# Kernel optimization log

Hardware: AMD Instinct MI355X
Metric: run time of the kernel (lower is better)

## Reference

```python
import jax, jax.numpy as jnp
import numpy as np

# ---- static config (matches init_kwargs) ----
B, NPG, C, L, H = 128, 256, 128, 3, 4   # graphs, nodes/graph, hidden, layers, heads
IN_CH, WALK, EDGE_IN, DEG = 30, 20, 11, 8
N = B * NPG
E = N * DEG
EPG = E // B                             # edges per graph
BN_EPS = 1e-5
HD = C // H


def setup_inputs() -> dict:
    key = jax.random.key(0)
    ks = list(jax.random.split(key, 80))
    ki = iter(ks)
    def w(shape, s=0.05):
        return jax.random.normal(next(ki), shape, jnp.float32) * s
    x = jax.random.normal(next(ki), (N, IN_CH), jnp.float32)
    # edges strictly within each graph (block-diagonal structure)
    src_l = jax.random.randint(next(ki), (E,), 0, NPG)
    dst_l = jax.random.randint(next(ki), (E,), 0, NPG)
    eg = jnp.repeat(jnp.arange(B, dtype=jnp.int32), EPG)
    edge_index = jnp.stack([eg * NPG + src_l.astype(jnp.int32),
                            eg * NPG + dst_l.astype(jnp.int32)])
    edge_attr = jax.random.normal(next(ki), (E, EDGE_IN), jnp.float32)
    batch = jnp.repeat(jnp.arange(B, dtype=jnp.int32), NPG)
    # all Linear weights stored [in, out] so y = x @ W + b
    inp = dict(x=x, edge_attr=edge_attr,
        in_W=w((IN_CH + WALK, C)), in_b=jnp.zeros((C,)),
        ep_W=w((EDGE_IN, C)), ep_b=jnp.zeros((C,)),
        ge_W=w((L, C, C)), ge_b=jnp.zeros((L, C)),          # GINE edge lin
        g1_W=w((L, C, C)), g1_b=jnp.zeros((L, C)),          # GINE nn layer1
        g2_W=w((L, C, C)), g2_b=jnp.zeros((L, C)),          # GINE nn layer2
        qkv_W=w((L, C, 3 * C)), qkv_b=jnp.zeros((L, 3 * C)),
        o_W=w((L, C, C)), o_b=jnp.zeros((L, C)),
        bn1_g=jnp.ones((L, C)), bn1_b=jnp.zeros((L, C)), bn1_m=w((L, C), 0.1), bn1_v=jnp.ones((L, C)),
        bn2_g=jnp.ones((L, C)), bn2_b=jnp.zeros((L, C)), bn2_m=w((L, C), 0.1), bn2_v=jnp.ones((L, C)),
        bn3_g=jnp.ones((L, C)), bn3_b=jnp.zeros((L, C)), bn3_m=w((L, C), 0.1), bn3_v=jnp.ones((L, C)),
        m1_W=w((L, C, 2 * C)), m1_b=jnp.zeros((L, 2 * C)),  # GPS ff block
        m2_W=w((L, 2 * C, C)), m2_b=jnp.zeros((L, C)),
        h1_W=w((C, 64)), h1_b=jnp.zeros((64,)),
        h2_W=w((64, 1)), h2_b=jnp.zeros((1,)),
        edge_index=edge_index, batch=batch)
    return inp


def _bn(x, g, b, m, v):  # BatchNorm1d, inference mode
    return (x - m) * jax.lax.rsqrt(v + BN_EPS) * g + b


def _rwse(edge_index):
    """diag of k-step random-walk matrix per graph; [N, WALK]."""
    src, dst = edge_index
    g = src // NPG
    A = jnp.zeros((B, NPG, NPG), jnp.float32).at[g, src % NPG, dst % NPG].add(1.0)
    A = A + jnp.eye(NPG, dtype=jnp.float32)          # add_self_loops
    deg = jnp.clip(jnp.sum(A, axis=-1), 1.0)         # out-degree of source
    M = jnp.swapaxes(A / deg[..., None], -1, -2)     # M[c,r] = A[r,c]/deg[r]
    p0 = jnp.broadcast_to(jnp.eye(NPG, dtype=jnp.float32), (B, NPG, NPG))
    def step(p, _):
        p = jnp.einsum('bcr,brn->bcn', M, p)
        return p, jnp.diagonal(p, axis1=-2, axis2=-1)
    _, diags = jax.lax.scan(step, p0, None, length=WALK)  # [WALK, B, NPG]
    return jnp.transpose(diags, (1, 2, 0)).reshape(N, WALK)


def _forward(x, edge_attr, in_W, in_b, ep_W, ep_b, ge_W, ge_b, g1_W, g1_b, g2_W, g2_b,
             qkv_W, qkv_b, o_W, o_b,
             bn1_g, bn1_b, bn1_m, bn1_v, bn2_g, bn2_b, bn2_m, bn2_v, bn3_g, bn3_b, bn3_m, bn3_v,
             m1_W, m1_b, m2_W, m2_b, h1_W, h1_b, h2_W, h2_b, edge_index, batch):
    pe = _rwse(edge_index)
    h = jnp.concatenate([x, pe], axis=-1) @ in_W + in_b      # input_proj
    e_emb = edge_attr @ ep_W + ep_b                          # edge_proj (dim==11)
    src, dst = edge_index[0], edge_index[1]
    for i in range(L):
        # --- GINEConv: relu(x_j + lin(edge)) -> scatter-sum -> MLP; eps=0 ---
        e = e_emb @ ge_W[i] + ge_b[i]
        msg = jax.nn.relu(h[src] + e)
        aggr = jax.ops.segment_sum(msg, dst, num_segments=N)
        loc = jax.nn.relu((h + aggr) @ g1_W[i] + g1_b[i]) @ g2_W[i] + g2_b[i]
        h1 = _bn(loc + h, bn1_g[i], bn1_b[i], bn1_m[i], bn1_v[i])
        # --- global multi-head attention on dense batch (uniform n, no padding) ---
        hd = h.reshape(B, NPG, C)
        qkv = hd @ qkv_W[i] + qkv_b[i]
        q, k, v = jnp.split(qkv, 3, axis=-1)
        q = q.reshape(B, NPG, H, HD); k = k.reshape(B, NPG, H, HD); v = v.reshape(B, NPG, H, HD)
        scores = jnp.einsum('bqhd,bkhd->bhqk', q, k) * (HD ** -0.5)
        attn = jax.nn.softmax(scores, axis=-1)
        o = jnp.einsum('bhqk,bkhd->bqhd', attn, v).reshape(B, NPG, C)
        o = (o @ o_W[i] + o_b[i]).reshape(N, C)
        h2 = _bn(o + h, bn2_g[i], bn2_b[i], bn2_m[i], bn2_v[i])
        # --- combine + feed-forward block ---
        out = h1 + h2
        ff = jax.nn.relu(out @ m1_W[i] + m1_b[i]) @ m2_W[i] + m2_b[i]
        h = _bn(out + ff, bn3_g[i], bn3_b[i], bn3_m[i], bn3_v[i])
    # --- global mean pool + head ---
    cnt = jax.ops.segment_sum(jnp.ones((N,), jnp.float32), batch, num_segments=B)
    pooled = jax.ops.segment_sum(h, batch, num_segments=B) / cnt[:, None]
    out = jax.nn.relu(pooled @ h1_W + h1_b) @ h2_W + h2_b
    return out[:, 0]  # [B]


def reference(x, edge_attr, in_W, in_b, ep_W, ep_b, ge_W, ge_b, g1_W, g1_b, g2_W, g2_b,
              qkv_W, qkv_b, o_W, o_b,
              bn1_g, bn1_b, bn1_m, bn1_v, bn2_g, bn2_b, bn2_m, bn2_v, bn3_g, bn3_b, bn3_m, bn3_v,
              m1_W, m1_b, m2_W, m2_b, h1_W, h1_b, h2_W, h2_b, edge_index, batch):
    return _forward(x, edge_attr, in_W, in_b, ep_W, ep_b, ge_W, ge_b, g1_W, g1_b, g2_W, g2_b,
                    qkv_W, qkv_b, o_W, o_b,
                    bn1_g, bn1_b, bn1_m, bn1_v, bn2_g, bn2_b, bn2_m, bn2_v, bn3_g, bn3_b, bn3_m, bn3_v,
                    m1_W, m1_b, m2_W, m2_b, h1_W, h1_b, h2_W, h2_b, edge_index, batch)
```

## Files before the change

### kernel.cpp

```cpp
#include <hip/hip_runtime.h>

#define GN   128
#define GP   256
#define NN   32768
#define NEDGE 262144
#define WALKN 20

typedef __attribute__((ext_vector_type(8))) short bfrag;
typedef __attribute__((ext_vector_type(4))) float ffrag;

__device__ __forceinline__ ushort f2b(float f){
  unsigned u = __float_as_uint(f);
  u += 0x7fffu + ((u >> 16) & 1u);
  return (ushort)(u >> 16);
}
__device__ __forceinline__ float b2f(ushort u){
  return __uint_as_float(((unsigned)u) << 16);
}
__device__ __forceinline__ unsigned addpair(unsigned a, unsigned b){
  float alo = __uint_as_float(a << 16), ahi = __uint_as_float(a & 0xffff0000u);
  float blo = __uint_as_float(b << 16), bhi = __uint_as_float(b & 0xffff0000u);
  return ((unsigned)f2b(ahi + bhi) << 16) | (unsigned)f2b(alo + blo);
}

__global__ __launch_bounds__(256) void build_edges(const int* __restrict__ ei, float* __restrict__ A,
                                                   int* __restrict__ epos, int* __restrict__ Ecnt){
  int e = blockIdx.x*256 + threadIdx.x;
  int s = ei[e], d = ei[NEDGE + e];
  int g = s >> 8;
  atomicAdd(&A[((size_t)g<<16) + ((size_t)(s&255)<<8) + (size_t)(d&255)], 1.0f);
  epos[e] = atomicAdd(&Ecnt[d], 1);
}

__global__ __launch_bounds__(256) void pack_edges(const int* __restrict__ ei, const float* __restrict__ ea,
                                                  const int* __restrict__ epos, float* __restrict__ pk){
  int e = blockIdx.x*256 + threadIdx.x;
  int d = ei[NEDGE + e];
  int pos = epos[e];
  if (pos >= 32) return;
  float* dst = pk + ((size_t)d*32 + pos)*12;
  dst[0] = __int_as_float(ei[e]);
  const float* s = ea + (size_t)e*11;
  #pragma unroll
  for (int t = 0; t < 11; t++) dst[1+t] = s[t];
}

__global__ __launch_bounds__(256) void rwse_deg(float* __restrict__ A, float* __restrict__ deg){
  int g = blockIdx.x, r = threadIdx.x;
  float* row = A + ((size_t)g<<16) + ((size_t)r<<8);
  row[r] += 1.0f;
  float s = 0.f;
  for (int c = 0; c < 256; c += 4){
    float4 v = *(const float4*)&row[c];
    s += v.x + v.y + v.z + v.w;
  }
  deg[(g<<8)+r] = fmaxf(s, 1.0f);
}

__global__ __launch_bounds__(256) void prep_m(const float* __restrict__ A, const float* __restrict__ deg,
                                              ushort* __restrict__ Mbf){
  __shared__ float As[64][65];
  __shared__ float Bs[64][65];
  __shared__ float invd[256];
  int g = blockIdx.x;
  const float* Ag = A + ((size_t)g<<16);
  int tid = threadIdx.x, tx = tid & 63, ty = tid >> 6;
  invd[tid] = 1.f / deg[(g<<8)+tid];
  ushort* Mg = Mbf + ((size_t)g<<16);
  const int pr[10] = {0,0,0,0,1,1,1,2,2,3};
  const int pc[10] = {0,1,2,3,1,2,3,2,3,3};
  for (int t = 0; t < 10; t++){
    int R0 = pr[t]*64, C0 = pc[t]*64;
    __syncthreads();
    #pragma unroll
    for (int i = 0; i < 16; i++){
      As[ty + i*4][tx] = Ag[(size_t)(R0 + ty + i*4)*256 + C0 + tx];
      Bs[ty + i*4][tx] = Ag[(size_t)(C0 + ty + i*4)*256 + R0 + tx];
    }
    __syncthreads();
    #pragma unroll
    for (int i = 0; i < 16; i++){
      int cl = ty + i*4;
      Mg[(size_t)(C0+cl)*256 + R0+tx] = f2b(As[tx][cl] * invd[R0+tx]);
      if (R0 != C0)
        Mg[(size_t)(R0+cl)*256 + C0+tx] = f2b(Bs[tx][cl] * invd[C0+tx]);
    }
  }
}

__global__ __launch_bounds__(256, 2) void rwse_mf(const ushort* __restrict__ Mbf,
                                                  float* __restrict__ pe){
  __shared__ __align__(16) ushort Pt[64*264];
  int bid = blockIdx.x;
  int g  = (bid & 7)*16 + (bid >> 5);
  int cb = ((bid >> 3) & 3) << 6;
  int tid = threadIdx.x, lane = tid & 63, w = tid >> 6;
  int l15 = lane & 15, quad = lane >> 4;
  const ushort* Mg = Mbf + ((size_t)g << 16);
  uint4 z4; z4.x = z4.y = z4.z = z4.w = 0u;
  for (int i = tid; i < 2112; i += 256) reinterpret_cast<uint4*>(Pt)[i] = z4;
  __syncthreads();
  if (tid < 64) Pt[tid*264 + cb + tid] = 0x3F80;
  __syncthreads();

  for (int s = 0; s < WALKN; s++){
    ffrag acc[4][4];
    #pragma unroll
    for (int mi = 0; mi < 4; mi++)
      #pragma unroll
      for (int n = 0; n < 4; n++) acc[mi][n] = (ffrag){0.f,0.f,0.f,0.f};
    for (int k0 = 0; k0 < 256; k0 += 32){
      bfrag a[4], b[4];
      #pragma unroll
      for (int mi = 0; mi < 4; mi++)
        a[mi] = *reinterpret_cast<const bfrag*>(&Mg[(size_t)(w*64 + mi*16 + l15)*256 + k0 + quad*8]);
      #pragma unroll
      for (int n = 0; n < 4; n++)
        b[n] = *reinterpret_cast<const bfrag*>(&Pt[(n*16 + l15)*264 + k0 + quad*8]);
      #pragma unroll
      for (int mi = 0; mi < 4; mi++)
        #pragma unroll
        for (int n = 0; n < 4; n++)
          acc[mi][n] = __builtin_amdgcn_mfma_f32_16x16x32_bf16(a[mi], b[n], acc[mi][n], 0, 0, 0);
    }
    __syncthreads();
    #pragma unroll
    for (int mi = 0; mi < 4; mi++){
      int rbase = w*64 + mi*16 + quad*4;
      #pragma unroll
      for (int n = 0; n < 4; n++){
        int cl = n*16 + l15;
        int dd = cb + cl - rbase;
        if (dd >= 0 && dd < 4){
          float dv = (dd==0)?acc[mi][n][0]:(dd==1)?acc[mi][n][1]:(dd==2)?acc[mi][n][2]:acc[mi][n][3];
          pe[(size_t)((g<<8) + cb + cl)*WALKN + s] = dv;
        }
        ushort4 pkk;
        pkk.x = f2b(acc[mi][n][0]); pkk.y = f2b(acc[mi][n][1]);
        pkk.z = f2b(acc[mi][n][2]); pkk.w = f2b(acc[mi][n][3]);
        *reinterpret_cast<ushort4*>(&Pt[cl*264 + rbase]) = pkk;
      }
    }
    __syncthreads();
  }
}

__global__ __launch_bounds__(256) void concat_kernel(const float* __restrict__ x, const float* __restrict__ pe,
                                                     ushort* __restrict__ xinb){
  int idx = blockIdx.x*256 + threadIdx.x;
  int row = idx >> 6, c = idx & 63;
  float v = 0.f;
  if (c < 30) v = x[(size_t)row*30 + c];
  else if (c < 50) v = pe[(size_t)row*20 + (c-30)];
  xinb[idx] = f2b(v);
}

__global__ __launch_bounds__(256) void prep_wt(const float* __restrict__ in_W, const float* __restrict__ g1_W,
                                               const float* __restrict__ g2_W, const float* __restrict__ qkv_W,
                                               const float* __restrict__ o_W, const float* __restrict__ m1_W,
                                               const float* __restrict__ m2_W, ushort* __restrict__ wt){
  int rgn = blockIdx.y;
  const float* src; int K, N, Kp; size_t dst;
  if (rgn == 0){ src = in_W; K=50; N=128; Kp=64; dst = 0; }
  else if (rgn <= 3){ int i=rgn-1;  src = g1_W + (size_t)i*16384; K=128; N=128; Kp=128; dst = 8192   + (size_t)i*16384; }
  else if (rgn <= 6){ int i=rgn-4;  src = g2_W + (size_t)i*16384; K=128; N=128; Kp=128; dst = 57344  + (size_t)i*16384; }
  else if (rgn <= 9){ int i=rgn-7;  src = qkv_W+ (size_t)i*49152; K=128; N=384; Kp=128; dst = 106496 + (size_t)i*49152; }
  else if (rgn <= 12){ int i=rgn-10; src = o_W  + (size_t)i*16384; K=128; N=128; Kp=128; dst = 253952 + (size_t)i*16384; }
  else if (rgn <= 15){ int i=rgn-13; src = m1_W + (size_t)i*32768; K=128; N=256; Kp=128; dst = 303104 + (size_t)i*32768; }
  else               { int i=rgn-16; src = m2_W + (size_t)i*32768; K=256; N=128; Kp=256; dst = 401408 + (size_t)i*32768; }
  int sz = N * Kp;
  int idx = blockIdx.x*256 + threadIdx.x;
  if (idx >= sz) return;
  int n = idx / Kp, kp = idx - n*Kp;
  float v = (kp < K) ? src[(size_t)kp*N + n] : 0.f;
  wt[dst + idx] = f2b(v);
}

template<int CINP>
__global__ __launch_bounds__(256, 2) void gemm_b(
    const ushort* __restrict__ X1, const ushort* __restrict__ WT,
    const float* __restrict__ bias, ushort* __restrict__ Y, int ldY, int colTiles)
{
  constexpr int XS = CINP + 8;
  __shared__ ushort XA[64 * XS];
  __shared__ ushort WS[128 * XS];
  int bt = blockIdx.x;
  int row0 = (bt / colTiles) * 64;
  int c0   = (bt % colTiles) * 128;
  int tid = threadIdx.x;
  int lane = tid & 63, wave = tid >> 6;
  int l15 = lane & 15, quad = lane >> 4;
  int wr = wave >> 1, wc = wave & 1;
  constexpr int C8 = CINP/8;

  #pragma unroll
  for (int it = 0; it < CINP/32; it++){
    int idx = tid + it*256;
    int r = idx / C8, c8 = (idx % C8)*8;
    *reinterpret_cast<uint4*>(&XA[r*XS + c8]) =
        *reinterpret_cast<const uint4*>(&X1[(size_t)(row0+r)*CINP + c8]);
  }
  #pragma unroll
  for (int it = 0; it < CINP/16; it++){
    int idx = tid + it*256;
    int n = idx / C8, c8 = (idx % C8)*8;
    *reinterpret_cast<uint4*>(&WS[n*XS + c8]) =
        *reinterpret_cast<const uint4*>(&WT[(size_t)(c0+n)*CINP + c8]);
  }
  __syncthreads();
  ffrag acc[2][4];
  #pragma unroll
  for (int m = 0; m < 2; m++)
    #pragma unroll
    for (int n = 0; n < 4; n++) acc[m][n] = (ffrag){0.f,0.f,0.f,0.f};
  #pragma unroll
  for (int ks = 0; ks < CINP/32; ks++){
    bfrag a[2], b[4];
    #pragma unroll
    for (int m = 0; m < 2; m++)
      a[m] = *reinterpret_cast<const bfrag*>(&XA[(32*wr + 16*m + l15)*XS + ks*32 + quad*8]);
    #pragma unroll
    for (int n = 0; n < 4; n++)
      b[n] = *reinterpret_cast<const bfrag*>(&WS[(64*wc + 16*n + l15)*XS + ks*32 + quad*8]);
    #pragma unroll
    for (int m = 0; m < 2; m++)
      #pragma unroll
      for (int n = 0; n < 4; n++)
        acc[m][n] = __builtin_amdgcn_mfma_f32_16x16x32_bf16(a[m], b[n], acc[m][n], 0, 0, 0);
  }
  #pragma unroll
  for (int m = 0; m < 2; m++)
    #pragma unroll
    for (int n = 0; n < 4; n++){
      int col = c0 + 64*wc + 16*n + l15;
      float bs = bias[col];
      #pragma unroll
      for (int rg = 0; rg < 4; rg++){
        int r = row0 + 32*wr + 16*m + quad*4 + rg;
        Y[(size_t)r*ldY + col] = f2b(acc[m][n][rg] + bs);
      }
    }
}

__global__ __launch_bounds__(256, 2) void gine_mlp(
    const ushort* __restrict__ hb, const ushort* __restrict__ agb,
    const ushort* __restrict__ w1, const float* __restrict__ b1v,
    const ushort* __restrict__ w2, const float* __restrict__ b2v,
    const float* __restrict__ bng, const float* __restrict__ bnb,
    const float* __restrict__ bnm, const float* __restrict__ bnv,
    ushort* __restrict__ h1b)
{
  __shared__ ushort XA[64*136];
  __shared__ ushort WS[128*136];
  __shared__ ushort T1[64*136];
  int row0 = blockIdx.x * 64;
  int tid = threadIdx.x, lane = tid & 63, wave = tid >> 6;
  int l15 = lane & 15, quad = lane >> 4;
  int wr = wave >> 1, wc = wave & 1;

  #pragma unroll
  for (int it = 0; it < 4; it++){
    int idx = tid + it*256;
    int r = idx >> 4, c8 = (idx & 15)*8;
    uint4 av = *reinterpret_cast<const uint4*>(&hb[(size_t)(row0+r)*128 + c8]);
    uint4 bv = *reinterpret_cast<const uint4*>(&agb[(size_t)(row0+r)*128 + c8]);
    uint4 o; o.x=addpair(av.x,bv.x); o.y=addpair(av.y,bv.y); o.z=addpair(av.z,bv.z); o.w=addpair(av.w,bv.w);
    *reinterpret_cast<uint4*>(&XA[r*136 + c8]) = o;
  }
  #pragma unroll
  for (int it = 0; it < 8; it++){
    int idx = tid + it*256;
    int n = idx >> 4, c8 = (idx & 15)*8;
    *reinterpret_cast<uint4*>(&WS[n*136 + c8]) =
        *reinterpret_cast<const uint4*>(&w1[(size_t)n*128 + c8]);
  }
  __syncthreads();
  ffrag acc[2][4];
  #pragma unroll
  for (int m = 0; m < 2; m++)
    #pragma unroll
    for (int n = 0; n < 4; n++) acc[m][n] = (ffrag){0.f,0.f,0.f,0.f};
  #pragma unroll
  for (int ks = 0; ks < 4; ks++){
    bfrag a[2], b[4];
    #pragma unroll
    for (int m = 0; m < 2; m++)
      a[m] = *reinterpret_cast<const bfrag*>(&XA[(32*wr + 16*m + l15)*136 + ks*32 + quad*8]);
    #pragma unroll
    for (int n = 0; n < 4; n++)
      b[n] = *reinterpret_cast<const bfrag*>(&WS[(64*wc + 16*n + l15)*136 + ks*32 + quad*8]);
    #pragma unroll
    for (int m = 0; m < 2; m++)
      #pragma unroll
      for (int n = 0; n < 4; n++)
        acc[m][n] = __builtin_amdgcn_mfma_f32_16x16x32_bf16(a[m], b[n], acc[m][n], 0, 0, 0);
  }
  __syncthreads();
  #pragma unroll
  for (int m = 0; m < 2; m++)
    #pragma unroll
    for (int n = 0; n < 4; n++){
      int col = 64*wc + 16*n + l15;
      float bs = b1v[col];
      #pragma unroll
      for (int rg = 0; rg < 4; rg++){
        int rl = 32*wr + 16*m + quad*4 + rg;
        T1[rl*136 + col] = f2b(fmaxf(acc[m][n][rg] + bs, 0.f));
      }
    }
  #pragma unroll
  for (int it = 0; it < 8; it++){
    int idx = tid + it*256;
    int n = idx >> 4, c8 = (idx & 15)*8;
    *reinterpret_cast<uint4*>(&WS[n*136 + c8]) =
        *reinterpret_cast<const uint4*>(&w2[(size_t)n*128 + c8]);
  }
  __syncthreads();
  #pragma unroll
  for (int m = 0; m < 2; m++)
    #pragma unroll
    for (int n = 0; n < 4; n++) acc[m][n] = (ffrag){0.f,0.f,0.f,0.f};
  #pragma unroll
  for (int ks = 0; ks < 4; ks++){
    bfrag a[2], b[4];
    #pragma unroll
    for (int m = 0; m < 2; m++)
      a[m] = *reinterpret_cast<const bfrag*>(&T1[(32*wr + 16*m + l15)*136 + ks*32 + quad*8]);
    #pragma unroll
    for (int n = 0; n < 4; n++)
      b[n] = *reinterpret_cast<const bfrag*>(&WS[(64*wc + 16*n + l15)*136 + ks*32 + quad*8]);
    #pragma unroll
    for (int m = 0; m < 2; m++)
      #pragma unroll
      for (int n = 0; n < 4; n++)
        acc[m][n] = __builtin_amdgcn_mfma_f32_16x16x32_bf16(a[m], b[n], acc[m][n], 0, 0, 0);
  }
  #pragma unroll
  for (int m = 0; m < 2; m++)
    #pragma unroll
    for (int n = 0; n < 4; n++){
      int col = 64*wc + 16*n + l15;
      float bs = b2v[col];
      float sc = rsqrtf(bnv[col] + 1e-5f) * bng[col];
      float sh = bnb[col] - bnm[col]*sc;
      #pragma unroll
      for (int rg = 0; rg < 4; rg++){
        int r = row0 + 32*wr + 16*m + quad*4 + rg;
        float v = acc[m][n][rg] + bs + b2f(hb[(size_t)r*128 + col]);
        h1b[(size_t)r*128 + col] = f2b(v*sc + sh);
      }
    }
}

__global__ __launch_bounds__(256, 1) void ff_fused(
    const ushort* __restrict__ obb, const ushort* __restrict__ hb, const ushort* __restrict__ h1b,
    const ushort* __restrict__ wo, const float* __restrict__ ob_b,
    const float* __restrict__ bn2g, const float* __restrict__ bn2b,
    const float* __restrict__ bn2m, const float* __restrict__ bn2v,
    const ushort* __restrict__ wm1, const float* __restrict__ m1b,
    const ushort* __restrict__ wm2, const float* __restrict__ m2b,
    const float* __restrict__ bn3g, const float* __restrict__ bn3b,
    const float* __restrict__ bn3m, const float* __restrict__ bn3v,
    ushort* __restrict__ hout)
{
  __shared__ ushort XA[64*136];
  __shared__ ushort WS[256*136];
  __shared__ ushort OUT[64*136];
  __shared__ ushort T2[64*264];
  int row0 = blockIdx.x * 64;
  int tid = threadIdx.x, lane = tid & 63, wave = tid >> 6;
  int l15 = lane & 15, quad = lane >> 4;
  int wr = wave >> 1, wc = wave & 1;

  #pragma unroll
  for (int it = 0; it < 4; it++){
    int idx = tid + it*256;
    int r = idx >> 4, c8 = (idx & 15)*8;
    *reinterpret_cast<uint4*>(&XA[r*136 + c8]) =
        *reinterpret_cast<const uint4*>(&obb[(size_t)(row0+r)*128 + c8]);
  }
  #pragma unroll
  for (int it = 0; it < 8; it++){
    int idx = tid + it*256;
    int n = idx >> 4, c8 = (idx & 15)*8;
    *reinterpret_cast<uint4*>(&WS[n*136 + c8]) =
        *reinterpret_cast<const uint4*>(&wo[(size_t)n*128 + c8]);
  }
  __syncthreads();
  ffrag acc[2][4];
  #pragma unroll
  for (int m = 0; m < 2; m++)
    #pragma unroll
    for (int n = 0; n < 4; n++) acc[m][n] = (ffrag){0.f,0.f,0.f,0.f};
  #pragma unroll
  for (int ks = 0; ks < 4; ks++){
    bfrag a[2], b[4];
    #pragma unroll
    for (int m = 0; m < 2; m++)
      a[m] = *reinterpret_cast<const bfrag*>(&XA[(32*wr + 16*m + l15)*136 + ks*32 + quad*8]);
    #pragma unroll
    for (int n = 0; n < 4; n++)
      b[n] = *reinterpret_cast<const bfrag*>(&WS[(64*wc + 16*n + l15)*136 + ks*32 + quad*8]);
    #pragma unroll
    for (int m = 0; m < 2; m++)
      #pragma unroll
      for (int n = 0; n < 4; n++)
        acc[m][n] = __builtin_amdgcn_mfma_f32_16x16x32_bf16(a[m], b[n], acc[m][n], 0, 0, 0);
  }
  __syncthreads();
  #pragma unroll
  for (int m = 0; m < 2; m++)
    #pragma unroll
    for (int n = 0; n < 4; n++){
      int col = 64*wc + 16*n + l15;
      float bs = ob_b[col];
      float sc = rsqrtf(bn2v[col] + 1e-5f) * bn2g[col];
      float sh = bn2b[col] - bn2m[col]*sc;
      #pragma unroll
      for (int rg = 0; rg < 4; rg++){
        int rl = 32*wr + 16*m + quad*4 + rg;
        int r = row0 + rl;
        float v = acc[m][n][rg] + bs + b2f(hb[(size_t)r*128 + col]);
        v = v*sc + sh + b2f(h1b[(size_t)r*128 + col]);
        OUT[rl*136 + col] = f2b(v);
      }
    }
  #pragma unroll
  for (int it = 0; it < 16; it++){
    int idx = tid + it*256;
    int n = idx >> 4, c8 = (idx & 15)*8;
    *reinterpret_cast<uint4*>(&WS[n*136 + c8]) =
        *reinterpret_cast<const uint4*>(&wm1[(size_t)n*128 + c8]);
  }
  __syncthreads();
  ffrag acc2[2][8];
  #pragma unroll
  for (int m = 0; m < 2; m++)
    #pragma unroll
    for (int n = 0; n < 8; n++) acc2[m][n] = (ffrag){0.f,0.f,0.f,0.f};
  #pragma unroll
  for (int ks = 0; ks < 4; ks++){
    bfrag a[2], b[8];
    #pragma unroll
    for (int m = 0; m < 2; m++)
      a[m] = *reinterpret_cast<const bfrag*>(&OUT[(32*wr + 16*m + l15)*136 + ks*32 + quad*8]);
    #pragma unroll
    for (int n = 0; n < 8; n++)
      b[n] = *reinterpret_cast<const bfrag*>(&WS[(128*wc + 16*n + l15)*136 + ks*32 + quad*8]);
    #pragma unroll
    for (int m = 0; m < 2; m++)
      #pragma unroll
      for (int n = 0; n < 8; n++)
        acc2[m][n] = __builtin_amdgcn_mfma_f32_16x16x32_bf16(a[m], b[n], acc2[m][n], 0, 0, 0);
  }
  __syncthreads();
  #pragma unroll
  for (int m = 0; m < 2; m++)
    #pragma unroll
    for (int n = 0; n < 8; n++){
      int col = 128*wc + 16*n + l15;
      float bs = m1b[col];
      #pragma unroll
      for (int rg = 0; rg < 4; rg++){
        int rl = 32*wr + 16*m + quad*4 + rg;
        T2[rl*264 + col] = f2b(fmaxf(acc2[m][n][rg] + bs, 0.f));
      }
    }
  #pragma unroll
  for (int it = 0; it < 16; it++){
    int idx = tid + it*256;
    int n = idx >> 5, c8 = (idx & 31)*8;
    *reinterpret_cast<uint4*>(&WS[n*264 + c8]) =
        *reinterpret_cast<const uint4*>(&wm2[(size_t)n*256 + c8]);
  }
  __syncthreads();
  #pragma unroll
  for (int m = 0; m < 2; m++)
    #pragma unroll
    for (int n = 0; n < 4; n++) acc[m][n] = (ffrag){0.f,0.f,0.f,0.f};
  #pragma unroll
  for (int ks = 0; ks < 8; ks++){
    bfrag a[2], b[4];
    #pragma unroll
    for (int m = 0; m < 2; m++)
      a[m] = *reinterpret_cast<const bfrag*>(&T2[(32*wr + 16*m + l15)*264 + ks*32 + quad*8]);
    #pragma unroll
    for (int n = 0; n < 4; n++)
      b[n] = *reinterpret_cast<const bfrag*>(&WS[(64*wc + 16*n + l15)*264 + ks*32 + quad*8]);
    #pragma unroll
    for (int m = 0; m < 2; m++)
      #pragma unroll
      for (int n = 0; n < 4; n++)
        acc[m][n] = __builtin_amdgcn_mfma_f32_16x16x32_bf16(a[m], b[n], acc[m][n], 0, 0, 0);
  }
  #pragma unroll
  for (int m = 0; m < 2; m++)
    #pragma unroll
    for (int n = 0; n < 4; n++){
      int col = 64*wc + 16*n + l15;
      float bs = m2b[col];
      float sc = rsqrtf(bn3v[col] + 1e-5f) * bn3g[col];
      float sh = bn3b[col] - bn3m[col]*sc;
      #pragma unroll
      for (int rg = 0; rg < 4; rg++){
        int rl = 32*wr + 16*m + quad*4 + rg;
        float v = acc[m][n][rg] + bs + b2f(OUT[rl*136 + col]);
        hout[(size_t)(row0+rl)*128 + col] = f2b(v*sc + sh);
      }
    }
}

__global__ __launch_bounds__(256) void wp_all(const float* __restrict__ epW, const float* __restrict__ epb,
                                              const float* __restrict__ geW, const float* __restrict__ geb,
                                              float* __restrict__ Wp, float* __restrict__ bp){
  int i = blockIdx.x;
  const float* gw = geW + (size_t)i*16384;
  float* wp = Wp + (size_t)i*1408;
  int tid = threadIdx.x;
  for (int idx = tid; idx < 1408; idx += 256){
    int t = idx >> 7, c = idx & 127;
    float s = 0.f;
    for (int k = 0; k < 128; k++) s += epW[t*128+k] * gw[(size_t)k*128 + c];
    wp[idx] = s;
  }
  if (tid < 128){
    float s = geb[(size_t)i*128 + tid];
    for (int k = 0; k < 128; k++) s += epb[k] * gw[(size_t)k*128 + tid];
    bp[(size_t)i*128 + tid] = s;
  }
}

__global__ __launch_bounds__(256) void gine_aggr2(const ushort* __restrict__ hb, const float* __restrict__ pk,
                                                  const int* __restrict__ Ecnt,
                                                  const float* __restrict__ Wp, const float* __restrict__ bp,
                                                  ushort* __restrict__ agb){
  int n = blockIdx.x*2 + (threadIdx.x >> 7);
  int ch = threadIdx.x & 127;
  int cnt = Ecnt[n]; if (cnt > 32) cnt = 32;
  float wreg[11];
  #pragma unroll
  for (int t = 0; t < 11; t++) wreg[t] = Wp[t*128 + ch];
  float bpc = bp[ch];
  const float* pkn = pk + (size_t)n*384;
  float acc = 0.f;
  int j = 0;
  for (; j + 4 <= cnt; j += 4){
    const float* p0 = pkn + (size_t)(j+0)*12;
    const float* p1 = pkn + (size_t)(j+1)*12;
    const float* p2 = pkn + (size_t)(j+2)*12;
    const float* p3 = pkn + (size_t)(j+3)*12;
    int s0 = __float_as_int(p0[0]), s1 = __float_as_int(p1[0]);
    int s2 = __float_as_int(p2[0]), s3 = __float_as_int(p3[0]);
    float h0 = b2f(hb[(size_t)s0*128 + ch]);
    float h1 = b2f(hb[(size_t)s1*128 + ch]);
    float h2 = b2f(hb[(size_t)s2*128 + ch]);
    float h3 = b2f(hb[(size_t)s3*128 + ch]);
    float e0 = bpc, e1 = bpc, e2 = bpc, e3 = bpc;
    #pragma unroll
    for (int t = 0; t < 11; t++){
      e0 += p0[1+t]*wreg[t]; e1 += p1[1+t]*wreg[t];
      e2 += p2[1+t]*wreg[t]; e3 += p3[1+t]*wreg[t];
    }
    acc += fmaxf(h0+e0, 0.f) + fmaxf(h1+e1, 0.f) + fmaxf(h2+e2, 0.f) + fmaxf(h3+e3, 0.f);
  }
  for (; j < cnt; j++){
    const float* p0 = pkn + (size_t)j*12;
    int s0 = __float_as_int(p0[0]);
    float h0 = b2f(hb[(size_t)s0*128 + ch]);
    float e0 = bpc;
    #pragma unroll
    for (int t = 0; t < 11; t++) e0 += p0[1+t]*wreg[t];
    acc += fmaxf(h0+e0, 0.f);
  }
  agb[(size_t)n*128 + ch] = f2b(acc);
}

__global__ __launch_bounds__(256, 2) void attn_mf(const ushort* __restrict__ qkvb, ushort* __restrict__ obb){
  __shared__ ushort Ks[256 * 40];
  __shared__ ushort Vt[32 * 264];
  __shared__ ushort PA[4 * 16 * 264];
  int g = blockIdx.x >> 2, hh = blockIdx.x & 3;
  int tid = threadIdx.x, lane = tid & 63, w = tid >> 6;
  int l15 = lane & 15, quad = lane >> 4;
  const ushort* base = qkvb + (size_t)(g<<8)*384;

  #pragma unroll
  for (int it = 0; it < 4; it++){
    int idx = tid + it*256;
    int key = idx >> 2, d8 = (idx & 3)*8;
    uint4 kv = *reinterpret_cast<const uint4*>(&base[(size_t)key*384 + 128 + hh*32 + d8]);
    *reinterpret_cast<uint4*>(&Ks[key*40 + d8]) = kv;
    uint4 vv = *reinterpret_cast<const uint4*>(&base[(size_t)key*384 + 256 + hh*32 + d8]);
    const ushort* vp = reinterpret_cast<const ushort*>(&vv);
    #pragma unroll
    for (int t = 0; t < 8; t++) Vt[(d8+t)*264 + key] = vp[t];
  }
  bfrag qf[4];
  #pragma unroll
  for (int qg = 0; qg < 4; qg++){
    int q = w*64 + qg*16 + l15;
    qf[qg] = *reinterpret_cast<const bfrag*>(&base[(size_t)q*384 + hh*32 + quad*8]);
  }
  __syncthreads();

  ushort* pw = &PA[w * 16 * 264];
  const float sc_ = 0.17677669529663687f;
  for (int qg = 0; qg < 4; qg++){
    ffrag sc[16];
    #pragma unroll
    for (int kg = 0; kg < 16; kg++){
      bfrag bk = *reinterpret_cast<const bfrag*>(&Ks[(kg*16 + l15)*40 + quad*8]);
      ffrag z = (ffrag){0.f,0.f,0.f,0.f};
      sc[kg] = __builtin_amdgcn_mfma_f32_16x16x32_bf16(qf[qg], bk, z, 0, 0, 0);
    }
    float inv_l[4];
    #pragma unroll
    for (int rg = 0; rg < 4; rg++){
      float m = sc[0][rg];
      #pragma unroll
      for (int kg = 1; kg < 16; kg++) m = fmaxf(m, sc[kg][rg]);
      #pragma unroll
      for (int off = 1; off < 16; off <<= 1) m = fmaxf(m, __shfl_xor(m, off, 16));
      float ssum = 0.f;
      #pragma unroll
      for (int kg = 0; kg < 16; kg++){
        float p = __expf((sc[kg][rg] - m) * sc_);
        sc[kg][rg] = p; ssum += p;
      }
      #pragma unroll
      for (int off = 1; off < 16; off <<= 1) ssum += __shfl_xor(ssum, off, 16);
      inv_l[rg] = 1.f / ssum;
    }
    #pragma unroll
    for (int kg = 0; kg < 16; kg++)
      #pragma unroll
      for (int rg = 0; rg < 4; rg++)
        pw[(quad*4 + rg)*264 + kg*16 + l15] = f2b(sc[kg][rg]);
    ffrag oa[2];
    oa[0] = (ffrag){0.f,0.f,0.f,0.f};
    oa[1] = (ffrag){0.f,0.f,0.f,0.f};
    #pragma unroll
    for (int ks = 0; ks < 8; ks++){
      bfrag pa = *reinterpret_cast<const bfrag*>(&pw[l15*264 + ks*32 + quad*8]);
      #pragma unroll
      for (int n16 = 0; n16 < 2; n16++){
        bfrag bv = *reinterpret_cast<const bfrag*>(&Vt[(n16*16 + l15)*264 + ks*32 + quad*8]);
        oa[n16] = __builtin_amdgcn_mfma_f32_16x16x32_bf16(pa, bv, oa[n16], 0, 0, 0);
      }
    }
    #pragma unroll
    for (int n16 = 0; n16 < 2; n16++)
      #pragma unroll
      for (int rg = 0; rg < 4; rg++){
        int q = w*64 + qg*16 + quad*4 + rg;
        int col = hh*32 + n16*16 + l15;
        obb[((size_t)(g<<8) + q)*128 + col] = f2b(oa[n16][rg] * inv_l[rg]);
      }
  }
}

__global__ __launch_bounds__(256) void head_kernel(const ushort* __restrict__ hb,
                                                   const float* __restrict__ W1, const float* __restrict__ b1,
                                                   const float* __restrict__ W2, const float* __restrict__ b2,
                                                   float* __restrict__ out){
  int g = blockIdx.x, tid = threadIdx.x;
  int c = tid & 127, half = tid >> 7;
  __shared__ float part[2][128];
  __shared__ float pool[128];
  __shared__ float hid[64];
  float s = 0.f;
  for (int n = half*128; n < half*128 + 128; n++)
    s += b2f(hb[(size_t)((g<<8)+n)*128 + c]);
  part[half][c] = s;
  __syncthreads();
  if (tid < 128) pool[tid] = (part[0][tid] + part[1][tid]) * (1.f/256.f);
  __syncthreads();
  if (tid < 64){
    float v = b1[tid];
    for (int k = 0; k < 128; k++) v += pool[k] * W1[k*64 + tid];
    hid[tid] = fmaxf(v, 0.f);
  }
  __syncthreads();
  if (tid == 0){
    float v = b2[0];
    for (int k = 0; k < 64; k++) v += hid[k] * W2[k];
    out[g] = v;
  }
}

extern "C" void kernel_launch(void* const* d_in, const int* in_sizes, int n_in,
                              void* d_out, int out_size, void* d_ws, size_t ws_size,
                              hipStream_t stream){
  (void)in_sizes; (void)n_in; (void)out_size; (void)ws_size;
  const float* x      = (const float*)d_in[0];
  const float* eattr  = (const float*)d_in[1];
  const float* in_W   = (const float*)d_in[2];
  const float* in_b   = (const float*)d_in[3];
  const float* ep_W   = (const float*)d_in[4];
  const float* ep_b   = (const float*)d_in[5];
  const float* ge_W   = (const float*)d_in[6];
  const float* ge_b   = (const float*)d_in[7];
  const float* g1_W   = (const float*)d_in[8];
  const float* g1_b   = (const float*)d_in[9];
  const float* g2_W   = (const float*)d_in[10];
  const float* g2_b   = (const float*)d_in[11];
  const float* qkv_W  = (const float*)d_in[12];
  const float* qkv_b  = (const float*)d_in[13];
  const float* o_W    = (const float*)d_in[14];
  const float* o_b    = (const float*)d_in[15];
  const float* bn1g = (const float*)d_in[16]; const float* bn1b = (const float*)d_in[17];
  const float* bn1m = (const float*)d_in[18]; const float* bn1v = (const float*)d_in[19];
  const float* bn2g = (const float*)d_in[20]; const float* bn2b = (const float*)d_in[21];
  const float* bn2m = (const float*)d_in[22]; const float* bn2v = (const float*)d_in[23];
  const float* bn3g = (const float*)d_in[24]; const float* bn3b = (const float*)d_in[25];
  const float* bn3m = (const float*)d_in[26]; const float* bn3v = (const float*)d_in[27];
  const float* m1_W = (const float*)d_in[28]; const float* m1_b = (const float*)d_in[29];
  const float* m2_W = (const float*)d_in[30]; const float* m2_b = (const float*)d_in[31];
  const float* h1_W = (const float*)d_in[32]; const float* h1_b = (const float*)d_in[33];
  const float* h2_W = (const float*)d_in[34]; const float* h2_b = (const float*)d_in[35];
  const int*   ei   = (const int*)d_in[36];
  float* out = (float*)d_out;
  float* ws  = (float*)d_ws;
  int*   wsi = (int*)d_ws;

  const size_t oA    = 0;
  const size_t oMbf  = 8388608;
  const size_t oPk   = 12582912;
  const size_t oDeg  = 25165824;
  const size_t oPe   = 25198592;
  const size_t oHb   = 25853952;
  const size_t oH1b  = 27951104;
  const size_t oBb   = 30048256;
  const size_t oWp   = 32145408;
  const size_t oBp   = 32149632;
  const size_t oEpos = 32150016;
  const size_t oEcnt = 32412160;
  const size_t oWT   = 32444928;
  ushort* wt   = (ushort*)(ws + oWT);
  ushort* mbf  = (ushort*)(ws + oMbf);
  ushort* xinb = (ushort*)(ws + 0);
  ushort* qkvb = (ushort*)(ws + 0);
  ushort* hb   = (ushort*)(ws + oHb);
  ushort* h1b  = (ushort*)(ws + oH1b);
  ushort* bbuf = (ushort*)(ws + oBb);

  hipMemsetAsync(ws + oA, 0, 8388608*sizeof(float), stream);
  hipMemsetAsync(wsi + oEcnt, 0, 32768*sizeof(int), stream);
  build_edges<<<NEDGE/256, 256, 0, stream>>>(ei, ws+oA, wsi+oEpos, wsi+oEcnt);
  pack_edges<<<NEDGE/256, 256, 0, stream>>>(ei, eattr, wsi+oEpos, ws+oPk);
  rwse_deg<<<GN, 256, 0, stream>>>(ws+oA, ws+oDeg);
  prep_m<<<GN, 256, 0, stream>>>(ws+oA, ws+oDeg, mbf);
  rwse_mf<<<GN*4, 256, 0, stream>>>(mbf, ws+oPe);

  prep_wt<<<dim3(192, 19), 256, 0, stream>>>(in_W, g1_W, g2_W, qkv_W, o_W, m1_W, m2_W, wt);

  concat_kernel<<<NN*64/256, 256, 0, stream>>>(x, ws+oPe, xinb);
  gemm_b<64><<<512, 256, 0, stream>>>(xinb, wt + 0, in_b, hb, 128, 1);

  wp_all<<<3, 256, 0, stream>>>(ep_W, ep_b, ge_W, ge_b, ws+oWp, ws+oBp);

  for (int i = 0; i < 3; i++){
    gine_aggr2<<<NN/2, 256, 0, stream>>>(hb, ws+oPk, wsi+oEcnt,
                                         ws+oWp + (size_t)i*1408, ws+oBp + (size_t)i*128, bbuf);
    gine_mlp<<<512, 256, 0, stream>>>(hb, bbuf,
        wt + 8192 + (size_t)i*16384, g1_b + (size_t)i*128,
        wt + 57344 + (size_t)i*16384, g2_b + (size_t)i*128,
        bn1g+(size_t)i*128, bn1b+(size_t)i*128, bn1m+(size_t)i*128, bn1v+(size_t)i*128,
        h1b);
    gemm_b<128><<<1536, 256, 0, stream>>>(hb, wt + 106496 + (size_t)i*49152,
                                          qkv_b + (size_t)i*384, qkvb, 384, 3);
    attn_mf<<<GN*4, 256, 0, stream>>>(qkvb, bbuf);
    ff_fused<<<512, 256, 0, stream>>>(bbuf, hb, h1b,
        wt + 253952 + (size_t)i*16384, o_b + (size_t)i*128,
        bn2g+(size_t)i*128, bn2b+(size_t)i*128, bn2m+(size_t)i*128, bn2v+(size_t)i*128,
        wt + 303104 + (size_t)i*32768, m1_b + (size_t)i*256,
        wt + 401408 + (size_t)i*32768, m2_b + (size_t)i*128,
        bn3g+(size_t)i*128, bn3b+(size_t)i*128, bn3m+(size_t)i*128, bn3v+(size_t)i*128,
        hb);
  }

  head_kernel<<<GN, 256, 0, stream>>>(hb, h1_W, h1_b, h2_W, h2_b, out);
}
```

Baseline: 737.7 us.

## Stage per-graph node features in LDS for GINE aggregation and fuse degree prep

GINE aggregation now runs one block per half-graph. Each block first copies the graph's 256x128 bf16 node features into shared memory, so neighbour gathers hit LDS instead of scattered global reads. Each thread handles two channels, reads the packed edge records with float4 loads, and processes two edges per iteration. The degree computation is also folded into the M-matrix prep kernel, which drops one launch and the degree buffer round trip. The cost is 64KB of shared memory per block and a much smaller grid (256 blocks), which lowers parallelism and occupancy. Each block also loads the whole graph's features even though it only produces half of the destination nodes.

```diff
diff --git a/kernel.cpp b/kernel.cpp
--- a/kernel.cpp
+++ b/kernel.cpp
@@ -45,27 +45,23 @@
   for (int t = 0; t < 11; t++) dst[1+t] = s[t];
 }
 
-__global__ __launch_bounds__(256) void rwse_deg(float* __restrict__ A, float* __restrict__ deg){
-  int g = blockIdx.x, r = threadIdx.x;
-  float* row = A + ((size_t)g<<16) + ((size_t)r<<8);
-  row[r] += 1.0f;
-  float s = 0.f;
-  for (int c = 0; c < 256; c += 4){
-    float4 v = *(const float4*)&row[c];
-    s += v.x + v.y + v.z + v.w;
-  }
-  deg[(g<<8)+r] = fmaxf(s, 1.0f);
-}
-
-__global__ __launch_bounds__(256) void prep_m(const float* __restrict__ A, const float* __restrict__ deg,
-                                              ushort* __restrict__ Mbf){
+__global__ __launch_bounds__(256) void prep_m2(float* __restrict__ A, ushort* __restrict__ Mbf){
   __shared__ float As[64][65];
   __shared__ float Bs[64][65];
   __shared__ float invd[256];
   int g = blockIdx.x;
-  const float* Ag = A + ((size_t)g<<16);
+  float* Ag = A + ((size_t)g<<16);
   int tid = threadIdx.x, tx = tid & 63, ty = tid >> 6;
-  invd[tid] = 1.f / deg[(g<<8)+tid];
+  {
+    float* row = Ag + ((size_t)tid<<8);
+    row[tid] += 1.0f;
+    float s = 0.f;
+    for (int c = 0; c < 256; c += 4){
+      float4 v = *(const float4*)&row[c];
+      s += v.x + v.y + v.z + v.w;
+    }
+    invd[tid] = 1.f / fmaxf(s, 1.0f);
+  }
   ushort* Mg = Mbf + ((size_t)g<<16);
   const int pr[10] = {0,0,0,0,1,1,1,2,2,3};
   const int pc[10] = {0,1,2,3,1,2,3,2,3,3};
@@ -530,49 +526,74 @@
   }
 }
 
-__global__ __launch_bounds__(256) void gine_aggr2(const ushort* __restrict__ hb, const float* __restrict__ pk,
-                                                  const int* __restrict__ Ecnt,
-                                                  const float* __restrict__ Wp, const float* __restrict__ bp,
-                                                  ushort* __restrict__ agb){
-  int n = blockIdx.x*2 + (threadIdx.x >> 7);
-  int ch = threadIdx.x & 127;
-  int cnt = Ecnt[n]; if (cnt > 32) cnt = 32;
-  float wreg[11];
-  #pragma unroll
-  for (int t = 0; t < 11; t++) wreg[t] = Wp[t*128 + ch];
-  float bpc = bp[ch];
-  const float* pkn = pk + (size_t)n*384;
-  float acc = 0.f;
-  int j = 0;
-  for (; j + 4 <= cnt; j += 4){
-    const float* p0 = pkn + (size_t)(j+0)*12;
-    const float* p1 = pkn + (size_t)(j+1)*12;
-    const float* p2 = pkn + (size_t)(j+2)*12;
-    const float* p3 = pkn + (size_t)(j+3)*12;
-    int s0 = __float_as_int(p0[0]), s1 = __float_as_int(p1[0]);
-    int s2 = __float_as_int(p2[0]), s3 = __float_as_int(p3[0]);
-    float h0 = b2f(hb[(size_t)s0*128 + ch]);
-    float h1 = b2f(hb[(size_t)s1*128 + ch]);
-    float h2 = b2f(hb[(size_t)s2*128 + ch]);
-    float h3 = b2f(hb[(size_t)s3*128 + ch]);
-    float e0 = bpc, e1 = bpc, e2 = bpc, e3 = bpc;
-    #pragma unroll
-    for (int t = 0; t < 11; t++){
-      e0 += p0[1+t]*wreg[t]; e1 += p1[1+t]*wreg[t];
-      e2 += p2[1+t]*wreg[t]; e3 += p3[1+t]*wreg[t];
-    }
-    acc += fmaxf(h0+e0, 0.f) + fmaxf(h1+e1, 0.f) + fmaxf(h2+e2, 0.f) + fmaxf(h3+e3, 0.f);
-  }
-  for (; j < cnt; j++){
-    const float* p0 = pkn + (size_t)j*12;
-    int s0 = __float_as_int(p0[0]);
-    float h0 = b2f(hb[(size_t)s0*128 + ch]);
-    float e0 = bpc;
-    #pragma unroll
-    for (int t = 0; t < 11; t++) e0 += p0[1+t]*wreg[t];
-    acc += fmaxf(h0+e0, 0.f);
-  }
-  agb[(size_t)n*128 + ch] = f2b(acc);
+__global__ __launch_bounds__(256, 2) void gine_aggr3(
+    const ushort* __restrict__ hb, const float* __restrict__ pk,
+    const int* __restrict__ Ecnt,
+    const float* __restrict__ Wp, const float* __restrict__ bp,
+    ushort* __restrict__ agb)
+{
+  __shared__ ushort Hs[256*128];
+  int g = blockIdx.x >> 1;
+  int half = blockIdx.x & 1;
+  int tid = threadIdx.x;
+  const ushort* hg = hb + ((size_t)(g<<8))*128;
+  #pragma unroll
+  for (int it = 0; it < 16; it++){
+    int idx = tid + it*256;
+    reinterpret_cast<uint4*>(Hs)[idx] = reinterpret_cast<const uint4*>(hg)[idx];
+  }
+  int sub = tid >> 6;
+  int cp  = tid & 63;
+  float w0[11], w1[11];
+  #pragma unroll
+  for (int t = 0; t < 11; t++){ w0[t] = Wp[t*128 + cp*2]; w1[t] = Wp[t*128 + cp*2 + 1]; }
+  float bp0 = bp[cp*2], bp1 = bp[cp*2 + 1];
+  __syncthreads();
+
+  for (int d0 = 0; d0 < 128; d0 += 4){
+    int dst = (g<<8) + half*128 + d0 + sub;
+    int cnt = Ecnt[dst]; if (cnt > 32) cnt = 32;
+    float a0 = 0.f, a1 = 0.f;
+    const float4* pr = reinterpret_cast<const float4*>(pk + (size_t)dst*384);
+    int j = 0;
+    for (; j + 2 <= cnt; j += 2){
+      float4 q0 = pr[j*3+0], q1 = pr[j*3+1], q2 = pr[j*3+2];
+      float4 r0 = pr[j*3+3], r1 = pr[j*3+4], r2 = pr[j*3+5];
+      int sA = __float_as_int(q0.x) & 255;
+      int sB = __float_as_int(r0.x) & 255;
+      unsigned hA = *reinterpret_cast<const unsigned*>(&Hs[sA*128 + cp*2]);
+      unsigned hB = *reinterpret_cast<const unsigned*>(&Hs[sB*128 + cp*2]);
+      float eA0 = bp0 + q0.y*w0[0] + q0.z*w0[1] + q0.w*w0[2]
+                + q1.x*w0[3] + q1.y*w0[4] + q1.z*w0[5] + q1.w*w0[6]
+                + q2.x*w0[7] + q2.y*w0[8] + q2.z*w0[9] + q2.w*w0[10];
+      float eA1 = bp1 + q0.y*w1[0] + q0.z*w1[1] + q0.w*w1[2]
+                + q1.x*w1[3] + q1.y*w1[4] + q1.z*w1[5] + q1.w*w1[6]
+                + q2.x*w1[7] + q2.y*w1[8] + q2.z*w1[9] + q2.w*w1[10];
+      float eB0 = bp0 + r0.y*w0[0] + r0.z*w0[1] + r0.w*w0[2]
+                + r1.x*w0[3] + r1.y*w0[4] + r1.z*w0[5] + r1.w*w0[6]
+                + r2.x*w0[7] + r2.y*w0[8] + r2.z*w0[9] + r2.w*w0[10];
+      float eB1 = bp1 + r0.y*w1[0] + r0.z*w1[1] + r0.w*w1[2]
+                + r1.x*w1[3] + r1.y*w1[4] + r1.z*w1[5] + r1.w*w1[6]
+                + r2.x*w1[7] + r2.y*w1[8] + r2.z*w1[9] + r2.w*w1[10];
+      a0 += fmaxf(eA0 + b2f((ushort)hA), 0.f) + fmaxf(eB0 + b2f((ushort)hB), 0.f);
+      a1 += fmaxf(eA1 + b2f((ushort)(hA >> 16)), 0.f) + fmaxf(eB1 + b2f((ushort)(hB >> 16)), 0.f);
+    }
+    for (; j < cnt; j++){
+      float4 q0 = pr[j*3+0], q1 = pr[j*3+1], q2 = pr[j*3+2];
+      int sA = __float_as_int(q0.x) & 255;
+      unsigned hA = *reinterpret_cast<const unsigned*>(&Hs[sA*128 + cp*2]);
+      float eA0 = bp0 + q0.y*w0[0] + q0.z*w0[1] + q0.w*w0[2]
+                + q1.x*w0[3] + q1.y*w0[4] + q1.z*w0[5] + q1.w*w0[6]
+                + q2.x*w0[7] + q2.y*w0[8] + q2.z*w0[9] + q2.w*w0[10];
+      float eA1 = bp1 + q0.y*w1[0] + q0.z*w1[1] + q0.w*w1[2]
+                + q1.x*w1[3] + q1.y*w1[4] + q1.z*w1[5] + q1.w*w1[6]
+                + q2.x*w1[7] + q2.y*w1[8] + q2.z*w1[9] + q2.w*w1[10];
+      a0 += fmaxf(eA0 + b2f((ushort)hA), 0.f);
+      a1 += fmaxf(eA1 + b2f((ushort)(hA >> 16)), 0.f);
+    }
+    unsigned o = ((unsigned)f2b(a1) << 16) | (unsigned)f2b(a0);
+    *reinterpret_cast<unsigned*>(&agb[(size_t)dst*128 + cp*2]) = o;
+  }
 }
 
 __global__ __launch_bounds__(256, 2) void attn_mf(const ushort* __restrict__ qkvb, ushort* __restrict__ obb){
@@ -726,7 +747,6 @@
   const size_t oA    = 0;
   const size_t oMbf  = 8388608;
   const size_t oPk   = 12582912;
-  const size_t oDeg  = 25165824;
   const size_t oPe   = 25198592;
   const size_t oHb   = 25853952;
   const size_t oH1b  = 27951104;
@@ -748,8 +768,7 @@
   hipMemsetAsync(wsi + oEcnt, 0, 32768*sizeof(int), stream);
   build_edges<<<NEDGE/256, 256, 0, stream>>>(ei, ws+oA, wsi+oEpos, wsi+oEcnt);
   pack_edges<<<NEDGE/256, 256, 0, stream>>>(ei, eattr, wsi+oEpos, ws+oPk);
-  rwse_deg<<<GN, 256, 0, stream>>>(ws+oA, ws+oDeg);
-  prep_m<<<GN, 256, 0, stream>>>(ws+oA, ws+oDeg, mbf);
+  prep_m2<<<GN, 256, 0, stream>>>(ws+oA, mbf);
   rwse_mf<<<GN*4, 256, 0, stream>>>(mbf, ws+oPe);
 
   prep_wt<<<dim3(192, 19), 256, 0, stream>>>(in_W, g1_W, g2_W, qkv_W, o_W, m1_W, m2_W, wt);
@@ -760,7 +779,7 @@
   wp_all<<<3, 256, 0, stream>>>(ep_W, ep_b, ge_W, ge_b, ws+oWp, ws+oBp);
 
   for (int i = 0; i < 3; i++){
-    gine_aggr2<<<NN/2, 256, 0, stream>>>(hb, ws+oPk, wsi+oEcnt,
+    gine_aggr3<<<GN*2, 256, 0, stream>>>(hb, ws+oPk, wsi+oEcnt,
                                          ws+oWp + (size_t)i*1408, ws+oBp + (size_t)i*128, bbuf);
     gine_mlp<<<512, 256, 0, stream>>>(hb, bbuf,
         wt + 8192 + (size_t)i*16384, g1_b + (size_t)i*128,
```

New measurement: 799.8 us. 8.4% more time.

## Fuse edge build/pack, degree/prep, concat/input GEMM; widen RWSE tiles

Applied to the files above, without the earlier changes.

Merges edge counting and packing into one kernel, folds the degree computation into the transition-matrix prep, and fuses the feature concat into a dedicated input GEMM. The random-walk MFMA kernel now uses 512-thread blocks covering 128 columns, halving the re-reads of M per graph. This removes several launches and intermediate buffers. The larger LDS footprint and register use in the RWSE kernel may lower occupancy.

```diff
diff --git a/kernel.cpp b/kernel.cpp
--- a/kernel.cpp
+++ b/kernel.cpp
@@ -23,49 +23,40 @@
   return ((unsigned)f2b(ahi + bhi) << 16) | (unsigned)f2b(alo + blo);
 }
 
-__global__ __launch_bounds__(256) void build_edges(const int* __restrict__ ei, float* __restrict__ A,
-                                                   int* __restrict__ epos, int* __restrict__ Ecnt){
+__global__ __launch_bounds__(256) void build_pack(const int* __restrict__ ei, const float* __restrict__ ea,
+                                                  float* __restrict__ A, int* __restrict__ Ecnt,
+                                                  float* __restrict__ pk){
   int e = blockIdx.x*256 + threadIdx.x;
   int s = ei[e], d = ei[NEDGE + e];
   int g = s >> 8;
   atomicAdd(&A[((size_t)g<<16) + ((size_t)(s&255)<<8) + (size_t)(d&255)], 1.0f);
-  epos[e] = atomicAdd(&Ecnt[d], 1);
-}
-
-__global__ __launch_bounds__(256) void pack_edges(const int* __restrict__ ei, const float* __restrict__ ea,
-                                                  const int* __restrict__ epos, float* __restrict__ pk){
-  int e = blockIdx.x*256 + threadIdx.x;
-  int d = ei[NEDGE + e];
-  int pos = epos[e];
-  if (pos >= 32) return;
-  float* dst = pk + ((size_t)d*32 + pos)*12;
-  dst[0] = __int_as_float(ei[e]);
-  const float* s = ea + (size_t)e*11;
-  #pragma unroll
-  for (int t = 0; t < 11; t++) dst[1+t] = s[t];
-}
-
-__global__ __launch_bounds__(256) void rwse_deg(float* __restrict__ A, float* __restrict__ deg){
-  int g = blockIdx.x, r = threadIdx.x;
-  float* row = A + ((size_t)g<<16) + ((size_t)r<<8);
-  row[r] += 1.0f;
-  float s = 0.f;
-  for (int c = 0; c < 256; c += 4){
-    float4 v = *(const float4*)&row[c];
-    s += v.x + v.y + v.z + v.w;
-  }
-  deg[(g<<8)+r] = fmaxf(s, 1.0f);
-}
-
-__global__ __launch_bounds__(256) void prep_m(const float* __restrict__ A, const float* __restrict__ deg,
-                                              ushort* __restrict__ Mbf){
+  int pos = atomicAdd(&Ecnt[d], 1);
+  if (pos < 32){
+    float* dst = pk + ((size_t)d*32 + pos)*12;
+    dst[0] = __int_as_float(s);
+    const float* src = ea + (size_t)e*11;
+    #pragma unroll
+    for (int t = 0; t < 11; t++) dst[1+t] = src[t];
+  }
+}
+
+__global__ __launch_bounds__(256) void prep_m2(float* __restrict__ A, ushort* __restrict__ Mbf){
   __shared__ float As[64][65];
   __shared__ float Bs[64][65];
   __shared__ float invd[256];
   int g = blockIdx.x;
-  const float* Ag = A + ((size_t)g<<16);
+  float* Ag = A + ((size_t)g<<16);
   int tid = threadIdx.x, tx = tid & 63, ty = tid >> 6;
-  invd[tid] = 1.f / deg[(g<<8)+tid];
+  {
+    float* row = Ag + ((size_t)tid<<8);
+    row[tid] += 1.0f;
+    float s = 0.f;
+    for (int c = 0; c < 256; c += 4){
+      float4 v = *(const float4*)&row[c];
+      s += v.x + v.y + v.z + v.w;
+    }
+    invd[tid] = 1.f / fmaxf(s, 1.0f);
+  }
   ushort* Mg = Mbf + ((size_t)g<<16);
   const int pr[10] = {0,0,0,0,1,1,1,2,2,3};
   const int pc[10] = {0,1,2,3,1,2,3,2,3,3};
@@ -88,47 +79,47 @@
   }
 }
 
-__global__ __launch_bounds__(256, 2) void rwse_mf(const ushort* __restrict__ Mbf,
+__global__ __launch_bounds__(512, 4) void rwse_mf(const ushort* __restrict__ Mbf,
                                                   float* __restrict__ pe){
-  __shared__ __align__(16) ushort Pt[64*264];
+  __shared__ __align__(16) ushort Pt[128*264];
   int bid = blockIdx.x;
-  int g  = (bid & 7)*16 + (bid >> 5);
-  int cb = ((bid >> 3) & 3) << 6;
+  int g  = (bid & 7)*16 + (bid >> 4);
+  int cb = ((bid >> 3) & 1) << 7;
   int tid = threadIdx.x, lane = tid & 63, w = tid >> 6;
   int l15 = lane & 15, quad = lane >> 4;
   const ushort* Mg = Mbf + ((size_t)g << 16);
   uint4 z4; z4.x = z4.y = z4.z = z4.w = 0u;
-  for (int i = tid; i < 2112; i += 256) reinterpret_cast<uint4*>(Pt)[i] = z4;
-  __syncthreads();
-  if (tid < 64) Pt[tid*264 + cb + tid] = 0x3F80;
+  for (int i = tid; i < 4224; i += 512) reinterpret_cast<uint4*>(Pt)[i] = z4;
+  __syncthreads();
+  if (tid < 128) Pt[tid*264 + cb + tid] = 0x3F80;
   __syncthreads();
 
   for (int s = 0; s < WALKN; s++){
-    ffrag acc[4][4];
-    #pragma unroll
-    for (int mi = 0; mi < 4; mi++)
-      #pragma unroll
-      for (int n = 0; n < 4; n++) acc[mi][n] = (ffrag){0.f,0.f,0.f,0.f};
+    ffrag acc[2][8];
+    #pragma unroll
+    for (int mi = 0; mi < 2; mi++)
+      #pragma unroll
+      for (int n = 0; n < 8; n++) acc[mi][n] = (ffrag){0.f,0.f,0.f,0.f};
     for (int k0 = 0; k0 < 256; k0 += 32){
-      bfrag a[4], b[4];
-      #pragma unroll
-      for (int mi = 0; mi < 4; mi++)
-        a[mi] = *reinterpret_cast<const bfrag*>(&Mg[(size_t)(w*64 + mi*16 + l15)*256 + k0 + quad*8]);
-      #pragma unroll
-      for (int n = 0; n < 4; n++)
+      bfrag a[2], b[8];
+      #pragma unroll
+      for (int mi = 0; mi < 2; mi++)
+        a[mi] = *reinterpret_cast<const bfrag*>(&Mg[(size_t)(w*32 + mi*16 + l15)*256 + k0 + quad*8]);
+      #pragma unroll
+      for (int n = 0; n < 8; n++)
         b[n] = *reinterpret_cast<const bfrag*>(&Pt[(n*16 + l15)*264 + k0 + quad*8]);
       #pragma unroll
-      for (int mi = 0; mi < 4; mi++)
+      for (int mi = 0; mi < 2; mi++)
         #pragma unroll
-        for (int n = 0; n < 4; n++)
+        for (int n = 0; n < 8; n++)
           acc[mi][n] = __builtin_amdgcn_mfma_f32_16x16x32_bf16(a[mi], b[n], acc[mi][n], 0, 0, 0);
     }
     __syncthreads();
     #pragma unroll
-    for (int mi = 0; mi < 4; mi++){
-      int rbase = w*64 + mi*16 + quad*4;
-      #pragma unroll
-      for (int n = 0; n < 4; n++){
+    for (int mi = 0; mi < 2; mi++){
+      int rbase = w*32 + mi*16 + quad*4;
+      #pragma unroll
+      for (int n = 0; n < 8; n++){
         int cl = n*16 + l15;
         int dd = cb + cl - rbase;
         if (dd >= 0 && dd < 4){
@@ -143,16 +134,6 @@
     }
     __syncthreads();
   }
-}
-
-__global__ __launch_bounds__(256) void concat_kernel(const float* __restrict__ x, const float* __restrict__ pe,
-                                                     ushort* __restrict__ xinb){
-  int idx = blockIdx.x*256 + threadIdx.x;
-  int row = idx >> 6, c = idx & 63;
-  float v = 0.f;
-  if (c < 30) v = x[(size_t)row*30 + c];
-  else if (c < 50) v = pe[(size_t)row*20 + (c-30)];
-  xinb[idx] = f2b(v);
 }
 
 __global__ __launch_bounds__(256) void prep_wt(const float* __restrict__ in_W, const float* __restrict__ g1_W,
@@ -174,6 +155,70 @@
   int n = idx / Kp, kp = idx - n*Kp;
   float v = (kp < K) ? src[(size_t)kp*N + n] : 0.f;
   wt[dst + idx] = f2b(v);
+}
+
+__global__ __launch_bounds__(256, 2) void gemm_in(
+    const float* __restrict__ x, const float* __restrict__ pe,
+    const ushort* __restrict__ WT, const float* __restrict__ bias,
+    ushort* __restrict__ Y)
+{
+  __shared__ ushort XA[64 * 72];
+  __shared__ ushort WS[128 * 72];
+  int row0 = blockIdx.x * 64;
+  int tid = threadIdx.x;
+  int lane = tid & 63, wave = tid >> 6;
+  int l15 = lane & 15, quad = lane >> 4;
+  int wr = wave >> 1, wc = wave & 1;
+
+  #pragma unroll
+  for (int it = 0; it < 16; it++){
+    int idx = tid + it*256;
+    int r = idx >> 6, c = idx & 63;
+    float v = 0.f;
+    if (c < 30) v = x[(size_t)(row0+r)*30 + c];
+    else if (c < 50) v = pe[(size_t)(row0+r)*20 + (c-30)];
+    XA[r*72 + c] = f2b(v);
+  }
+  #pragma unroll
+  for (int it = 0; it < 4; it++){
+    int idx = tid + it*256;
+    int n = idx >> 3, c8 = (idx & 7)*8;
+    *reinterpret_cast<uint4*>(&WS[n*72 + c8]) =
+        *reinterpret_cast<const uint4*>(&WT[(size_t)n*64 + c8]);
+  }
+  __syncthreads();
+  ffrag acc[2][4];
+  #pragma unroll
+  for (int m = 0; m < 2; m++)
+    #pragma unroll
+    for (int n = 0; n < 4; n++) acc[m][n] = (ffrag){0.f,0.f,0.f,0.f};
+  #pragma unroll
+  for (int ks = 0; ks < 2; ks++){
+    bfrag a[2], b[4];
+    #pragma unroll
+    for (int m = 0; m < 2; m++)
+      a[m] = *reinterpret_cast<const bfrag*>(&XA[(32*wr + 16*m + l15)*72 + ks*32 + quad*8]);
+    #pragma unroll
+    for (int n = 0; n < 4; n++)
+      b[n] = *reinterpret_cast<const bfrag*>(&WS[(64*wc + 16*n + l15)*72 + ks*32 + quad*8]);
+    #pragma unroll
+    for (int m = 0; m < 2; m++)
+      #pragma unroll
+      for (int n = 0; n < 4; n++)
+        acc[m][n] = __builtin_amdgcn_mfma_f32_16x16x32_bf16(a[m], b[n], acc[m][n], 0, 0, 0);
+  }
+  #pragma unroll
+  for (int m = 0; m < 2; m++)
+    #pragma unroll
+    for (int n = 0; n < 4; n++){
+      int col = 64*wc + 16*n + l15;
+      float bs = bias[col];
+      #pragma unroll
+      for (int rg = 0; rg < 4; rg++){
+        int r = row0 + 32*wr + 16*m + quad*4 + rg;
+        Y[(size_t)r*128 + col] = f2b(acc[m][n][rg] + bs);
+      }
+    }
 }
 
 template<int CINP>
@@ -726,19 +771,16 @@
   const size_t oA    = 0;
   const size_t oMbf  = 8388608;
   const size_t oPk   = 12582912;
-  const size_t oDeg  = 25165824;
   const size_t oPe   = 25198592;
   const size_t oHb   = 25853952;
   const size_t oH1b  = 27951104;
   const size_t oBb   = 30048256;
   const size_t oWp   = 32145408;
   const size_t oBp   = 32149632;
-  const size_t oEpos = 32150016;
   const size_t oEcnt = 32412160;
   const size_t oWT   = 32444928;
   ushort* wt   = (ushort*)(ws + oWT);
   ushort* mbf  = (ushort*)(ws + oMbf);
-  ushort* xinb = (ushort*)(ws + 0);
   ushort* qkvb = (ushort*)(ws + 0);
   ushort* hb   = (ushort*)(ws + oHb);
   ushort* h1b  = (ushort*)(ws + oH1b);
@@ -746,16 +788,13 @@
 
   hipMemsetAsync(ws + oA, 0, 8388608*sizeof(float), stream);
   hipMemsetAsync(wsi + oEcnt, 0, 32768*sizeof(int), stream);
-  build_edges<<<NEDGE/256, 256, 0, stream>>>(ei, ws+oA, wsi+oEpos, wsi+oEcnt);
-  pack_edges<<<NEDGE/256, 256, 0, stream>>>(ei, eattr, wsi+oEpos, ws+oPk);
-  rwse_deg<<<GN, 256, 0, stream>>>(ws+oA, ws+oDeg);
-  prep_m<<<GN, 256, 0, stream>>>(ws+oA, ws+oDeg, mbf);
-  rwse_mf<<<GN*4, 256, 0, stream>>>(mbf, ws+oPe);
+  build_pack<<<NEDGE/256, 256, 0, stream>>>(ei, eattr, ws+oA, wsi+oEcnt, ws+oPk);
+  prep_m2<<<GN, 256, 0, stream>>>(ws+oA, mbf);
+  rwse_mf<<<GN*2, 512, 0, stream>>>(mbf, ws+oPe);
 
   prep_wt<<<dim3(192, 19), 256, 0, stream>>>(in_W, g1_W, g2_W, qkv_W, o_W, m1_W, m2_W, wt);
 
-  concat_kernel<<<NN*64/256, 256, 0, stream>>>(x, ws+oPe, xinb);
-  gemm_b<64><<<512, 256, 0, stream>>>(xinb, wt + 0, in_b, hb, 128, 1);
+  gemm_in<<<512, 256, 0, stream>>>(x, ws+oPe, wt + 0, in_b, hb);
 
   wp_all<<<3, 256, 0, stream>>>(ep_W, ep_b, ge_W, ge_b, ws+oWp, ws+oBp);
 
```

After: 839.5 us. 13.8% more time.
